# Optimization experiments

Measured on AMD Instinct MI355X. Metric: run time of the kernel, lower is better.

The kernel has to match this reference:

```python
import jax, jax.numpy as jnp
import numpy as np

KERNEL_SIZE = 10
PAD_LEFT = (KERNEL_SIZE - 1) // 2      # 4  (torch padding='same', even kernel)
PAD_RIGHT = (KERNEL_SIZE - 1) - PAD_LEFT  # 5


def setup_inputs() -> dict:
    key = jax.random.key(0)
    k1, _ = jax.random.split(key)
    n_bins, dim = 2048, 32768
    densities = jax.random.uniform(k1, (n_bins, dim), dtype=jnp.float32)
    bins = jnp.arange(n_bins, dtype=jnp.float32)  # uniform bin edges, width = 1.0
    return {"densities": densities, "bins": bins}


def reference(densities, bins):
    # densities: (n_bins, dim). The torch module transposes to (dim, n_bins) and
    # applies a per-channel uniform box filter of size KERNEL_SIZE with
    # replicate ('edge') padding. Diagonal-only conv == moving average, which we
    # implement with a cumsum sliding window (O(dim*n_bins) instead of O(dim^2*n_bins)).
    x = densities.T  # (dim, n_bins)
    xp = jnp.pad(x, ((0, 0), (PAD_LEFT, PAD_RIGHT)), mode="edge")  # (dim, n_bins+k-1)
    c = jnp.cumsum(xp, axis=-1)
    c0 = jnp.pad(c, ((0, 0), (1, 0)))  # prepend zero for window-sum differencing
    smoothed = (c0[:, KERNEL_SIZE:] - c0[:, :-KERNEL_SIZE]) / KERNEL_SIZE  # (dim, n_bins)
    smoothed = smoothed.T  # (n_bins, dim)
    # normalize each per-dim density to integrate to 1 over the bins
    width = bins[1] - bins[0]
    smoothed = smoothed / (smoothed * width).sum(axis=0)[None]
    return smoothed
```

## Files before the change

kernel.cpp:

```cpp
#include <hip/hip_runtime.h>


constexpr int NB   = 2048;
constexpr int DIM  = 32768;
constexpr int DIM4 = DIM / 4;

constexpr int W4     = 32;
constexpr int NBLK   = DIM4 / W4;
constexpr int NTHR   = 1024;
constexpr int RG     = NTHR / W4;
constexpr int ROWS   = NB / RG;

typedef float v4f __attribute__((ext_vector_type(4)));

__device__ __forceinline__ int clampb(int j) { return min(max(j, 0), NB - 1); }

__device__ __forceinline__ float wrow(int i) {
    int a = min(i + 4, NB - 1) - max(i - 5, 0) + 1;
    if (i == 0)      a += 10;
    if (i == NB - 1) a += 15;
    return (float)a;
}

__global__ __launch_bounds__(NTHR, 4) void k_onepass(const float* __restrict__ x,
                                                     const float* __restrict__ bins,
                                                     float* __restrict__ out) {
    const int t  = threadIdx.x;
    const int c  = t & (W4 - 1);
    const int rg = t >> 5;
    const int d4 = blockIdx.x * W4 + c;
    const int b0 = rg * ROWS;
    const v4f* __restrict__ px = reinterpret_cast<const v4f*>(x) + d4;

    __shared__ v4f sums[RG][W4];

    {
        v4f acc = {0.f, 0.f, 0.f, 0.f};
        if (rg == 0 || rg == RG - 1) {
            #pragma unroll 8
            for (int i = b0; i < b0 + ROWS; ++i)
                acc += wrow(i) * px[(size_t)i * DIM4];
        } else {
            #pragma unroll 8
            for (int i = b0; i < b0 + ROWS; ++i)
                acc += px[(size_t)i * DIM4];
            acc *= 10.f;
        }
        sums[rg][c] = acc;
    }
    __syncthreads();

    #pragma unroll
    for (int s = RG / 2; s > 0; s >>= 1) {
        if (rg < s) sums[rg][c] += sums[rg + s][c];
        __syncthreads();
    }

    const float width = bins[1] - bins[0];
    const v4f wsum = sums[0][c];
    v4f sc;
    sc.x = 1.f / (width * wsum.x);
    sc.y = 1.f / (width * wsum.y);
    sc.z = 1.f / (width * wsum.z);
    sc.w = 1.f / (width * wsum.w);

    v4f* __restrict__ po = reinterpret_cast<v4f*>(out) + d4;

    v4f prev[10], cur[10];
    #pragma unroll
    for (int m = 0; m < 10; ++m)
        prev[m] = px[(size_t)clampb(b0 - 4 + m) * DIM4];
    v4f S = prev[0];
    #pragma unroll
    for (int m = 1; m < 10; ++m) S += prev[m];

    constexpr int MAIN = ROWS - (ROWS % 10);
    for (int t0 = 0; t0 < MAIN; t0 += 10) {
        #pragma unroll
        for (int m = 0; m < 10; ++m)
            cur[m] = px[(size_t)min(b0 + t0 + m + 6, NB - 1) * DIM4];
        #pragma unroll
        for (int m = 0; m < 10; ++m) {
            v4f o = S * sc;
            __builtin_nontemporal_store(o, po + (size_t)(b0 + t0 + m) * DIM4);
            S += cur[m] - prev[m];
            prev[m] = cur[m];
        }
    }
    #pragma unroll
    for (int m = 0; m < ROWS % 10; ++m)
        cur[m] = px[(size_t)min(b0 + MAIN + m + 6, NB - 1) * DIM4];
    #pragma unroll
    for (int m = 0; m < ROWS % 10; ++m) {
        v4f o = S * sc;
        __builtin_nontemporal_store(o, po + (size_t)(b0 + MAIN + m) * DIM4);
        S += cur[m] - prev[m];
    }
}

extern "C" void kernel_launch(void* const* d_in, const int* in_sizes, int n_in,
                              void* d_out, int out_size, void* d_ws, size_t ws_size,
                              hipStream_t stream) {
    const float* x    = (const float*)d_in[0];
    const float* bins = (const float*)d_in[1];
    float* out = (float*)d_out;
    k_onepass<<<dim3(NBLK), dim3(NTHR), 0, stream>>>(x, bins, out);
}
```

Before: 124.0 us.

## Pipeline column-sum of second half-tile with smoothing pass of first half

Splits each block's 32-column tile into two 16-column halves handled by 64 row groups. The normalization sum for the second half is accumulated while the first half's smoothed output is written, which hides the separate reduction read phase behind streaming stores. Rows per thread halve to 32, and register use grows with the extra a1 buffer. Each half's data is still read twice, and coalescing drops to 256-byte segments per row.

```diff
diff --git a/kernel.cpp b/kernel.cpp
--- a/kernel.cpp
+++ b/kernel.cpp
@@ -1,15 +1,16 @@
 #include <hip/hip_runtime.h>
 
 
-constexpr int NB   = 2048;
-constexpr int DIM  = 32768;
-constexpr int DIM4 = DIM / 4;
+constexpr int NB    = 2048;
+constexpr int DIM   = 32768;
+constexpr int DIM4  = DIM / 4;
 
-constexpr int W4     = 32;
-constexpr int NBLK   = DIM4 / W4;
-constexpr int NTHR   = 1024;
-constexpr int RG     = NTHR / W4;
-constexpr int ROWS   = NB / RG;
+constexpr int W4    = 32;
+constexpr int H4    = 16;
+constexpr int NBLK  = DIM4 / W4;
+constexpr int NTHR  = 1024;
+constexpr int RGH   = NTHR / H4;
+constexpr int ROWSH = NB / RGH;
 
 typedef float v4f __attribute__((ext_vector_type(4)));
 
@@ -22,78 +23,138 @@
     return (float)a;
 }
 
-__global__ __launch_bounds__(NTHR, 4) void k_onepass(const float* __restrict__ x,
-                                                     const float* __restrict__ bins,
-                                                     float* __restrict__ out) {
-    const int t  = threadIdx.x;
-    const int c  = t & (W4 - 1);
-    const int rg = t >> 5;
-    const int d4 = blockIdx.x * W4 + c;
-    const int b0 = rg * ROWS;
-    const v4f* __restrict__ px = reinterpret_cast<const v4f*>(x) + d4;
+__global__ __launch_bounds__(NTHR, 4) void k_pipe(const float* __restrict__ x,
+                                                  const float* __restrict__ bins,
+                                                  float* __restrict__ out) {
+    const int t   = threadIdx.x;
+    const int ch  = t & (H4 - 1);
+    const int rgh = t >> 4;
+    const int b0  = rgh * ROWSH;
+    const size_t col0 = (size_t)blockIdx.x * W4 + ch;
+    const v4f* __restrict__ px0 = reinterpret_cast<const v4f*>(x) + col0;
+    const v4f* __restrict__ px1 = px0 + H4;
+    v4f* __restrict__ po0 = reinterpret_cast<v4f*>(out) + col0;
+    v4f* __restrict__ po1 = po0 + H4;
 
-    __shared__ v4f sums[RG][W4];
+    __shared__ v4f sums[RGH][H4];
+    const bool edge = (rgh == 0) || (rgh == RGH - 1);
+    constexpr int MAINH = ROWSH - (ROWSH % 10);
+    constexpr int TAILH = ROWSH % 10;
 
     {
         v4f acc = {0.f, 0.f, 0.f, 0.f};
-        if (rg == 0 || rg == RG - 1) {
+        if (edge) {
             #pragma unroll 8
-            for (int i = b0; i < b0 + ROWS; ++i)
-                acc += wrow(i) * px[(size_t)i * DIM4];
+            for (int i = b0; i < b0 + ROWSH; ++i)
+                acc += wrow(i) * px0[(size_t)i * DIM4];
         } else {
             #pragma unroll 8
-            for (int i = b0; i < b0 + ROWS; ++i)
-                acc += px[(size_t)i * DIM4];
+            for (int i = b0; i < b0 + ROWSH; ++i)
+                acc += px0[(size_t)i * DIM4];
             acc *= 10.f;
         }
-        sums[rg][c] = acc;
+        sums[rgh][ch] = acc;
     }
     __syncthreads();
-
     #pragma unroll
-    for (int s = RG / 2; s > 0; s >>= 1) {
-        if (rg < s) sums[rg][c] += sums[rg + s][c];
+    for (int s = RGH / 2; s > 0; s >>= 1) {
+        if (rgh < s) sums[rgh][ch] += sums[rgh + s][ch];
         __syncthreads();
     }
+    const float width = bins[1] - bins[0];
+    v4f sc0;
+    {
+        const v4f ws = sums[0][ch];
+        sc0.x = 1.f / (width * ws.x);
+        sc0.y = 1.f / (width * ws.y);
+        sc0.z = 1.f / (width * ws.z);
+        sc0.w = 1.f / (width * ws.w);
+    }
 
-    const float width = bins[1] - bins[0];
-    const v4f wsum = sums[0][c];
-    v4f sc;
-    sc.x = 1.f / (width * wsum.x);
-    sc.y = 1.f / (width * wsum.y);
-    sc.z = 1.f / (width * wsum.z);
-    sc.w = 1.f / (width * wsum.w);
-
-    v4f* __restrict__ po = reinterpret_cast<v4f*>(out) + d4;
-
-    v4f prev[10], cur[10];
+    v4f acc1 = {0.f, 0.f, 0.f, 0.f};
+    v4f prev[10], cur[10], a1[10];
     #pragma unroll
     for (int m = 0; m < 10; ++m)
-        prev[m] = px[(size_t)clampb(b0 - 4 + m) * DIM4];
+        prev[m] = px0[(size_t)clampb(b0 - 4 + m) * DIM4];
     v4f S = prev[0];
     #pragma unroll
     for (int m = 1; m < 10; ++m) S += prev[m];
 
-    constexpr int MAIN = ROWS - (ROWS % 10);
-    for (int t0 = 0; t0 < MAIN; t0 += 10) {
+    for (int t0 = 0; t0 < MAINH; t0 += 10) {
         #pragma unroll
         for (int m = 0; m < 10; ++m)
-            cur[m] = px[(size_t)min(b0 + t0 + m + 6, NB - 1) * DIM4];
+            cur[m] = px0[(size_t)min(b0 + t0 + m + 6, NB - 1) * DIM4];
+        #pragma unroll
+        for (int m = 0; m < 10; ++m)
+            a1[m] = px1[(size_t)(b0 + t0 + m) * DIM4];
         #pragma unroll
         for (int m = 0; m < 10; ++m) {
-            v4f o = S * sc;
-            __builtin_nontemporal_store(o, po + (size_t)(b0 + t0 + m) * DIM4);
+            v4f o = S * sc0;
+            __builtin_nontemporal_store(o, po0 + (size_t)(b0 + t0 + m) * DIM4);
+            S += cur[m] - prev[m];
+            prev[m] = cur[m];
+            if (edge) acc1 += wrow(b0 + t0 + m) * a1[m];
+            else      acc1 += a1[m];
+        }
+    }
+    #pragma unroll
+    for (int m = 0; m < TAILH; ++m) {
+        cur[m] = px0[(size_t)min(b0 + MAINH + m + 6, NB - 1) * DIM4];
+        a1[m]  = px1[(size_t)(b0 + MAINH + m) * DIM4];
+    }
+    #pragma unroll
+    for (int m = 0; m < TAILH; ++m) {
+        v4f o = S * sc0;
+        __builtin_nontemporal_store(o, po0 + (size_t)(b0 + MAINH + m) * DIM4);
+        S += cur[m] - prev[m];
+        if (edge) acc1 += wrow(b0 + MAINH + m) * a1[m];
+        else      acc1 += a1[m];
+    }
+    if (!edge) acc1 *= 10.f;
+
+    __syncthreads();
+    sums[rgh][ch] = acc1;
+    __syncthreads();
+    #pragma unroll
+    for (int s = RGH / 2; s > 0; s >>= 1) {
+        if (rgh < s) sums[rgh][ch] += sums[rgh + s][ch];
+        __syncthreads();
+    }
+    v4f sc1;
+    {
+        const v4f ws = sums[0][ch];
+        sc1.x = 1.f / (width * ws.x);
+        sc1.y = 1.f / (width * ws.y);
+        sc1.z = 1.f / (width * ws.z);
+        sc1.w = 1.f / (width * ws.w);
+    }
+
+    #pragma unroll
+    for (int m = 0; m < 10; ++m)
+        prev[m] = px1[(size_t)clampb(b0 - 4 + m) * DIM4];
+    S = prev[0];
+    #pragma unroll
+    for (int m = 1; m < 10; ++m) S += prev[m];
+
+    for (int t0 = 0; t0 < MAINH; t0 += 10) {
+        #pragma unroll
+        for (int m = 0; m < 10; ++m)
+            cur[m] = px1[(size_t)min(b0 + t0 + m + 6, NB - 1) * DIM4];
+        #pragma unroll
+        for (int m = 0; m < 10; ++m) {
+            v4f o = S * sc1;
+            __builtin_nontemporal_store(o, po1 + (size_t)(b0 + t0 + m) * DIM4);
             S += cur[m] - prev[m];
             prev[m] = cur[m];
         }
     }
     #pragma unroll
-    for (int m = 0; m < ROWS % 10; ++m)
-        cur[m] = px[(size_t)min(b0 + MAIN + m + 6, NB - 1) * DIM4];
+    for (int m = 0; m < TAILH; ++m)
+        cur[m] = px1[(size_t)min(b0 + MAINH + m + 6, NB - 1) * DIM4];
     #pragma unroll
-    for (int m = 0; m < ROWS % 10; ++m) {
-        v4f o = S * sc;
-        __builtin_nontemporal_store(o, po + (size_t)(b0 + MAIN + m) * DIM4);
+    for (int m = 0; m < TAILH; ++m) {
+        v4f o = S * sc1;
+        __builtin_nontemporal_store(o, po1 + (size_t)(b0 + MAINH + m) * DIM4);
         S += cur[m] - prev[m];
     }
 }
@@ -104,5 +165,5 @@
     const float* x    = (const float*)d_in[0];
     const float* bins = (const float*)d_in[1];
     float* out = (float*)d_out;
-    k_onepass<<<dim3(NBLK), dim3(NTHR), 0, stream>>>(x, bins, out);
+    k_pipe<<<dim3(NBLK), dim3(NTHR), 0, stream>>>(x, bins, out);
 }
```

Measured after the change: 198.2 us. +59.9%, slower.

## Hold row tile in registers, exchange halos via shuffles and LDS

Applied to the files above, without the earlier changes.

Each thread now loads its 16 rows once into registers. Those registers feed both the normalisation sum and the sliding-window pass, so the input is no longer read a second time from global memory. Neighbouring halo rows come from wave shuffles within a wave and from shared memory across wave boundaries. Blocks shrink to 8 float4 columns with 128 row groups, which deepens the reduction tree and raises register pressure.

```diff
diff --git a/kernel.cpp b/kernel.cpp
--- a/kernel.cpp
+++ b/kernel.cpp
@@ -5,15 +5,14 @@
 constexpr int DIM  = 32768;
 constexpr int DIM4 = DIM / 4;
 
-constexpr int W4     = 32;
-constexpr int NBLK   = DIM4 / W4;
-constexpr int NTHR   = 1024;
-constexpr int RG     = NTHR / W4;
-constexpr int ROWS   = NB / RG;
+constexpr int W4   = 8;
+constexpr int NBLK = DIM4 / W4;
+constexpr int NTHR = 1024;
+constexpr int RG   = NTHR / W4;
+constexpr int RT   = NB / RG;
+constexpr int NW   = NTHR / 64;
 
 typedef float v4f __attribute__((ext_vector_type(4)));
-
-__device__ __forceinline__ int clampb(int j) { return min(max(j, 0), NB - 1); }
 
 __device__ __forceinline__ float wrow(int i) {
     int a = min(i + 4, NB - 1) - max(i - 5, 0) + 1;
@@ -22,31 +21,58 @@
     return (float)a;
 }
 
-__global__ __launch_bounds__(NTHR, 4) void k_onepass(const float* __restrict__ x,
+__device__ __forceinline__ v4f shfl4(v4f v, int srcLane) {
+    v4f r;
+    r.x = __shfl(v.x, srcLane, 64);
+    r.y = __shfl(v.y, srcLane, 64);
+    r.z = __shfl(v.z, srcLane, 64);
+    r.w = __shfl(v.w, srcLane, 64);
+    return r;
+}
+
+__global__ __launch_bounds__(NTHR, 4) void k_regpass(const float* __restrict__ x,
                                                      const float* __restrict__ bins,
                                                      float* __restrict__ out) {
-    const int t  = threadIdx.x;
-    const int c  = t & (W4 - 1);
-    const int rg = t >> 5;
-    const int d4 = blockIdx.x * W4 + c;
-    const int b0 = rg * ROWS;
-    const v4f* __restrict__ px = reinterpret_cast<const v4f*>(x) + d4;
+    const int t    = threadIdx.x;
+    const int c    = t & (W4 - 1);
+    const int rg   = t >> 3;
+    const int lane = t & 63;
+    const int wave = t >> 6;
+    const int rgw  = (lane >> 3);
+    const int r0   = rg * RT;
+    const v4f* __restrict__ px = reinterpret_cast<const v4f*>(x)
+                                 + ((size_t)blockIdx.x * W4 + c);
+    v4f* __restrict__ po = reinterpret_cast<v4f*>(out)
+                           + ((size_t)blockIdx.x * W4 + c);
 
     __shared__ v4f sums[RG][W4];
+    __shared__ v4f pub_hi[NW][W4][4];
+    __shared__ v4f pub_lo[NW][W4][5];
+
+    v4f xv[RT];
+    #pragma unroll
+    for (int i = 0; i < RT; ++i)
+        xv[i] = px[(size_t)(r0 + i) * DIM4];
 
     {
         v4f acc = {0.f, 0.f, 0.f, 0.f};
         if (rg == 0 || rg == RG - 1) {
-            #pragma unroll 8
-            for (int i = b0; i < b0 + ROWS; ++i)
-                acc += wrow(i) * px[(size_t)i * DIM4];
+            #pragma unroll
+            for (int i = 0; i < RT; ++i) acc += wrow(r0 + i) * xv[i];
         } else {
-            #pragma unroll 8
-            for (int i = b0; i < b0 + ROWS; ++i)
-                acc += px[(size_t)i * DIM4];
+            #pragma unroll
+            for (int i = 0; i < RT; ++i) acc += xv[i];
             acc *= 10.f;
         }
         sums[rg][c] = acc;
+    }
+    if (rgw == 7) {
+        #pragma unroll
+        for (int j = 0; j < 4; ++j) pub_hi[wave][c][j] = xv[12 + j];
+    }
+    if (rgw == 0) {
+        #pragma unroll
+        for (int j = 0; j < 5; ++j) pub_lo[wave][c][j] = xv[j];
     }
     __syncthreads();
 
@@ -55,46 +81,47 @@
         if (rg < s) sums[rg][c] += sums[rg + s][c];
         __syncthreads();
     }
+    const float width = bins[1] - bins[0];
+    v4f sc;
+    {
+        const v4f ws = sums[0][c];
+        sc.x = 1.f / (width * ws.x);
+        sc.y = 1.f / (width * ws.y);
+        sc.z = 1.f / (width * ws.z);
+        sc.w = 1.f / (width * ws.w);
+    }
 
-    const float width = bins[1] - bins[0];
-    const v4f wsum = sums[0][c];
-    v4f sc;
-    sc.x = 1.f / (width * wsum.x);
-    sc.y = 1.f / (width * wsum.y);
-    sc.z = 1.f / (width * wsum.z);
-    sc.w = 1.f / (width * wsum.w);
-
-    v4f* __restrict__ po = reinterpret_cast<v4f*>(out) + d4;
-
-    v4f prev[10], cur[10];
-    #pragma unroll
-    for (int m = 0; m < 10; ++m)
-        prev[m] = px[(size_t)clampb(b0 - 4 + m) * DIM4];
-    v4f S = prev[0];
-    #pragma unroll
-    for (int m = 1; m < 10; ++m) S += prev[m];
-
-    constexpr int MAIN = ROWS - (ROWS % 10);
-    for (int t0 = 0; t0 < MAIN; t0 += 10) {
+    v4f b[4];
+    {
+        const int wlo = (wave > 0) ? wave - 1 : 0;
         #pragma unroll
-        for (int m = 0; m < 10; ++m)
-            cur[m] = px[(size_t)min(b0 + t0 + m + 6, NB - 1) * DIM4];
-        #pragma unroll
-        for (int m = 0; m < 10; ++m) {
-            v4f o = S * sc;
-            __builtin_nontemporal_store(o, po + (size_t)(b0 + t0 + m) * DIM4);
-            S += cur[m] - prev[m];
-            prev[m] = cur[m];
+        for (int j = 0; j < 4; ++j) {
+            v4f s = shfl4(xv[12 + j], (lane - 8) & 63);
+            v4f l = pub_hi[wlo][c][j];
+            b[j] = (rgw == 0) ? ((rg == 0) ? xv[0] : l) : s;
         }
     }
+
+    v4f S = b[0] + b[1] + b[2] + b[3]
+          + xv[0] + xv[1] + xv[2] + xv[3] + xv[4] + xv[5];
+
+    const int whi = (wave < NW - 1) ? wave + 1 : NW - 1;
     #pragma unroll
-    for (int m = 0; m < ROWS % 10; ++m)
-        cur[m] = px[(size_t)min(b0 + MAIN + m + 6, NB - 1) * DIM4];
-    #pragma unroll
-    for (int m = 0; m < ROWS % 10; ++m) {
+    for (int r = 0; r < RT; ++r) {
         v4f o = S * sc;
-        __builtin_nontemporal_store(o, po + (size_t)(b0 + MAIN + m) * DIM4);
-        S += cur[m] - prev[m];
+        __builtin_nontemporal_store(o, po + (size_t)(r0 + r) * DIM4);
+        if (r < RT - 1) {
+            v4f nx;
+            if (r < 10) {
+                nx = xv[r + 6];
+            } else {
+                v4f s = shfl4(xv[r - 10], (lane + 8) & 63);
+                v4f l = pub_lo[whi][c][r - 10];
+                nx = (rgw == 7) ? ((rg == RG - 1) ? xv[15] : l) : s;
+            }
+            v4f dp = (r >= 4) ? xv[r - 4] : b[r];
+            S += nx - dp;
+        }
     }
 }
 
@@ -104,5 +131,5 @@
     const float* x    = (const float*)d_in[0];
     const float* bins = (const float*)d_in[1];
     float* out = (float*)d_out;
-    k_onepass<<<dim3(NBLK), dim3(NTHR), 0, stream>>>(x, bins, out);
+    k_regpass<<<dim3(NBLK), dim3(NTHR), 0, stream>>>(x, bins, out);
 }
```

Result: faster. 106.0 us, median of 2 (-14.5%).
